# Performance work log

Measured on AMD Instinct MI355X. Metric: run time of the kernel, lower is better.

The kernel has to match this reference:

```python
import jax, jax.numpy as jnp
import numpy as np

ATTN_MULT = 8.0
NEG_INF = float('-inf')

N, Q, S, D = 16, 2048, 2048, 64


def setup_inputs() -> dict:
    key = jax.random.key(0)
    kq, kk, kv, kp = jax.random.split(key, 4)
    return {
        "queries_nqd": jax.random.normal(kq, (N, Q, D), dtype=jnp.float32),
        "keys_nsd": jax.random.normal(kk, (N, S, D), dtype=jnp.float32),
        "values_nsv": jax.random.normal(kv, (N, S, D), dtype=jnp.float32),
        "prefix_len_n": jax.random.randint(kp, (N,), 0, S, dtype=jnp.int64 if jax.config.jax_enable_x64 else jnp.int32),
    }


def reference(queries_nqd, keys_nsd, values_nsv, prefix_len_n):
    # attention_type == 'block_diagonal', backend == 'torch', dropout p == 0
    n, q, d = queries_nqd.shape
    s = keys_nsd.shape[1]
    scale = ATTN_MULT / d
    # prefix-block mask: key position < prefix_len (broadcast over queries)
    block_mask_n1s = (jnp.arange(s)[None, None, :] < prefix_len_n[:, None, None])  # [n,1,s]
    diag_mask_qs = jnp.arange(q)[:, None] == jnp.arange(s)[None, :]                # [q,s]
    mask_nqs = block_mask_n1s | diag_mask_qs[None, :, :]                           # [n,q,s]
    scores_nqs = jnp.einsum('nqd,nsd->nqs', queries_nqd, keys_nsd) * scale
    scores_nqs = jnp.where(mask_nqs, scores_nqs, NEG_INF)
    probs_nqs = jax.nn.softmax(scores_nqs, axis=-1)
    return jnp.einsum('nqs,nsv->nqv', probs_nqs, values_nsv)
```

## Files before the change

kernel.cpp:

```cpp
#include <hip/hip_runtime.h>
#include <hip/hip_bf16.h>
#include <math.h>

#define NH 16
#define QL 2048
#define SL 2048
#define DD 64
#define BQ 128
#define NSPLIT 2
#define PSTR 72
#define QK_SCALE_LOG2E 0.1803368801111f

typedef __attribute__((ext_vector_type(8))) short short8;
typedef __attribute__((ext_vector_type(4))) float floatx4;
typedef __attribute__((ext_vector_type(4))) unsigned short ushort4v;
typedef __attribute__((ext_vector_type(8))) unsigned short ushort8v;

__device__ __forceinline__ unsigned short f2bf(float x) {
    unsigned u = __float_as_uint(x);
    u += 0x7FFFu + ((u >> 16) & 1u);
    return (unsigned short)(u >> 16);
}
__device__ __forceinline__ unsigned int f2bf2u(float x, float y) {
    __hip_bfloat162 h = __float22bfloat162_rn(make_float2(x, y));
    return *(unsigned int*)&h;
}
__device__ __forceinline__ float bf2f(unsigned short h) {
    return __uint_as_float((unsigned)h << 16);
}

__device__ __forceinline__ void gld16(const unsigned short* g, unsigned short* l) {
    __builtin_amdgcn_global_load_lds(
        (const __attribute__((address_space(1))) unsigned int*)g,
        (__attribute__((address_space(3))) unsigned int*)l, 16, 0, 0);
}

__global__ __launch_bounds__(512) void k_prep(
    const float* __restrict__ Kf, const float* __restrict__ Vf,
    unsigned short* __restrict__ Kb, unsigned short* __restrict__ Vtb)
{
    __shared__ unsigned short sT[64][PSTR];
    const int bx = (int)blockIdx.x, tid = (int)threadIdx.x;

    const int gidx = bx * 512 + tid;
    #pragma unroll
    for (int k = 0; k < 2; ++k) {
        int idx = gidx + k * (512 * 512);
        float4 v = ((const float4*)Kf)[idx];
        ushort4v h = { f2bf(v.x), f2bf(v.y), f2bf(v.z), f2bf(v.w) };
        *(ushort4v*)(Kb + (size_t)idx * 4) = h;
    }

    const int n = bx >> 5, s0 = (bx & 31) * 64;
    const float* vb = Vf + ((size_t)n * SL + s0) * DD;
    #pragma unroll
    for (int i = 0; i < 2; ++i) {
        int idx = tid + i * 512;
        int r = idx >> 4, c = (idx & 15) << 2;
        float4 v = *(const float4*)(vb + r * DD + c);
        sT[c + 0][r] = f2bf(v.x);
        sT[c + 1][r] = f2bf(v.y);
        sT[c + 2][r] = f2bf(v.z);
        sT[c + 3][r] = f2bf(v.w);
    }
    __syncthreads();
    const int d = tid >> 3, sg = tid & 7;
    unsigned short* out = Vtb + (size_t)n * DD * SL + (size_t)d * SL + s0 + sg * 8;
    ushort8v a;
    #pragma unroll
    for (int i = 0; i < 8; ++i) a[i] = sT[d][sg * 8 + i];
    *(ushort8v*)out = a;
}

__global__ __launch_bounds__(512, 4) void k_attn(
    const float* __restrict__ Qf, const unsigned short* __restrict__ Kb,
    const unsigned short* __restrict__ Vtb, const int* __restrict__ plen_g,
    unsigned short* __restrict__ Opb, float* __restrict__ Lp)
{
    __shared__ unsigned short sK[3][64 * 64];
    __shared__ unsigned short sVt[3][64 * 64];
    __shared__ unsigned short sP[8 * 16 * 64];

    const int flat = (int)blockIdx.x;
    const int sp   = flat >> 8;
    const int rb   = flat & 255;
    const int n    = (rb + sp) & (NH - 1);
    const int qt   = rb >> 4;
    const int q0   = qt * BQ;
    const int plen = plen_g[n];

    const int tid  = (int)threadIdx.x;
    const int wave = tid >> 6, lane = tid & 63, quad = lane >> 4, l16 = lane & 15;

    const int ptiles = (plen + 63) >> 6;
    const int d0     = q0 >> 6;
    const int tdiag  = d0 + sp;
    const int cnt_p  = (ptiles + 1 - sp) >> 1;
    const int total  = cnt_p + (tdiag >= ptiles ? 1 : 0);

    const int qrow  = wave * 16 + l16;
    const int qglob = q0 + qrow;
    const int pmask = (l16 & 7) * 8;

    const unsigned short* kh = Kb  + (size_t)n * SL * DD;
    const unsigned short* vh = Vtb + (size_t)n * DD * SL;

    const int srow = wave * 8 + (lane >> 3);
    const int scol = ((lane & 7) ^ (srow & 7)) * 8;

    auto tile_of = [&](int i) -> int {
        return (i < cnt_p) ? (sp + (i << 1)) : tdiag;
    };
    auto stage = [&](int t, int b) {
        const unsigned short* kg = kh + ((size_t)t << 6) * DD;
        const unsigned short* vg = vh + (t << 6);
        gld16(kg + srow * DD + scol, sK[b] + wave * 512);
        gld16(vg + (size_t)srow * SL + scol, sVt[b] + wave * 512);
    };

    short8 bQ0, bQ1;
    {
        const float* qf = Qf + ((size_t)(n * QL + qglob)) * DD + quad * 8;
        float4 a0 = *(const float4*)(qf);
        float4 a1 = *(const float4*)(qf + 4);
        float4 c0 = *(const float4*)(qf + 32);
        float4 c1 = *(const float4*)(qf + 36);
        const float S = QK_SCALE_LOG2E;
        unsigned int u0[4] = {
            f2bf2u(a0.x * S, a0.y * S), f2bf2u(a0.z * S, a0.w * S),
            f2bf2u(a1.x * S, a1.y * S), f2bf2u(a1.z * S, a1.w * S) };
        unsigned int u1[4] = {
            f2bf2u(c0.x * S, c0.y * S), f2bf2u(c0.z * S, c0.w * S),
            f2bf2u(c1.x * S, c1.y * S), f2bf2u(c1.z * S, c1.w * S) };
        bQ0 = *(short8*)u0;
        bQ1 = *(short8*)u1;
    }

    stage(tile_of(0), 0);
    if (total > 1) stage(tile_of(1), 1);

    floatx4 acc[4];
    #pragma unroll
    for (int dt = 0; dt < 4; ++dt) acc[dt] = (floatx4){0.f, 0.f, 0.f, 0.f};
    float lsum = 0.f;
    unsigned short* pw = sP + qrow * 64;

    int bi = 0;
    int bs = 2;
    for (int i = 0; i < total; ++i) {
        if (i + 2 <= total) {
            asm volatile("s_waitcnt vmcnt(2) lgkmcnt(0)" ::: "memory");
        } else {
            asm volatile("s_waitcnt vmcnt(0) lgkmcnt(0)" ::: "memory");
        }
        __builtin_amdgcn_s_barrier();

        if (i + 2 < total) stage(tile_of(i + 2), bs);

        const unsigned short* sk = sK[bi];
        const unsigned short* sv = sVt[bi];
        const int t  = tile_of(i);
        const int s0 = t << 6;

        floatx4 sf[4];
        #pragma unroll
        for (int st2 = 0; st2 < 4; ++st2) sf[st2] = (floatx4){0.f, 0.f, 0.f, 0.f};
        __builtin_amdgcn_s_setprio(1);
        #pragma unroll
        for (int st2 = 0; st2 < 4; ++st2) {
            int krow = st2 * 16 + l16;
            short8 aK0 = *(const short8*)(sk + krow * 64 + (((0 * 4 + quad) ^ (krow & 7)) * 8));
            short8 aK1 = *(const short8*)(sk + krow * 64 + (((1 * 4 + quad) ^ (krow & 7)) * 8));
            sf[st2] = __builtin_amdgcn_mfma_f32_16x16x32_bf16(aK0, bQ0, sf[st2], 0, 0, 0);
            sf[st2] = __builtin_amdgcn_mfma_f32_16x16x32_bf16(aK1, bQ1, sf[st2], 0, 0, 0);
        }
        __builtin_amdgcn_s_setprio(0);

        if (s0 + 64 <= plen) {
            #pragma unroll
            for (int st2 = 0; st2 < 4; ++st2) {
                float p0 = __builtin_amdgcn_exp2f(sf[st2][0]);
                float p1 = __builtin_amdgcn_exp2f(sf[st2][1]);
                float p2 = __builtin_amdgcn_exp2f(sf[st2][2]);
                float p3 = __builtin_amdgcn_exp2f(sf[st2][3]);
                lsum += (p0 + p1) + (p2 + p3);
                uint2 pk = { f2bf2u(p0, p1), f2bf2u(p2, p3) };
                *(uint2*)(pw + ((st2 * 16 + quad * 4) ^ pmask)) = pk;
            }
        } else {
            #pragma unroll
            for (int st2 = 0; st2 < 4; ++st2) {
                float p[4];
                #pragma unroll
                for (int r2 = 0; r2 < 4; ++r2) {
                    int s = s0 + st2 * 16 + quad * 4 + r2;
                    bool valid = (s < plen) || (s == qglob);
                    p[r2] = __builtin_amdgcn_exp2f(valid ? sf[st2][r2] : -INFINITY);
                    lsum += p[r2];
                }
                uint2 pk = { f2bf2u(p[0], p[1]), f2bf2u(p[2], p[3]) };
                *(uint2*)(pw + ((st2 * 16 + quad * 4) ^ pmask)) = pk;
            }
        }

        __builtin_amdgcn_s_setprio(1);
        #pragma unroll
        for (int ks = 0; ks < 2; ++ks) {
            short8 aP = *(const short8*)(pw + ((ks * 32 + quad * 8) ^ pmask));
            #pragma unroll
            for (int dt = 0; dt < 4; ++dt) {
                int vrow = dt * 16 + l16;
                short8 bV = *(const short8*)(sv + vrow * 64 + (((ks * 4 + quad) ^ (vrow & 7)) * 8));
                acc[dt] = __builtin_amdgcn_mfma_f32_16x16x32_bf16(aP, bV, acc[dt], 0, 0, 0);
            }
        }
        __builtin_amdgcn_s_setprio(0);

        bi = (bi == 2) ? 0 : bi + 1;
        bs = (bs == 2) ? 0 : bs + 1;
    }

    lsum += __shfl_xor(lsum, 16, 64);
    lsum += __shfl_xor(lsum, 32, 64);
    if (quad == 0)
        Lp[((size_t)sp * NH + n) * QL + q0 + qrow] = lsum;

    unsigned short* pws = sP + wave * 16 * 64;
    #pragma unroll
    for (int dt = 0; dt < 4; ++dt) {
        int chunk = dt * 2 + (l16 >> 3);
        #pragma unroll
        for (int r2 = 0; r2 < 4; ++r2) {
            int row = quad * 4 + r2;
            int sw = ((chunk ^ (row & 7)) * 8) + (l16 & 7);
            pws[row * 64 + sw] = f2bf(acc[dt][r2]);
        }
    }
    const size_t qbase = ((size_t)sp * NH + n) * QL + q0 + wave * 16;
    #pragma unroll
    for (int t2 = 0; t2 < 2; ++t2) {
        int row = t2 * 8 + (lane >> 3);
        int chunk = lane & 7;
        int sw = (chunk ^ (row & 7)) * 8;
        ushort8v val = *(const ushort8v*)(pws + row * 64 + sw);
        *(ushort8v*)(Opb + (qbase + row) * DD + chunk * 8) = val;
    }
}

__global__ __launch_bounds__(512) void k_combine(
    const unsigned short* __restrict__ Opb, const float* __restrict__ Lp,
    float* __restrict__ Og)
{
    const int idx = (int)(blockIdx.x * 512 + threadIdx.x);
    const int d8 = idx & 7;
    const int q  = (idx >> 3) & (QL - 1);
    const int n  = idx >> 14;
    float s[8];
    #pragma unroll
    for (int j = 0; j < 8; ++j) s[j] = 0.f;
    float l = 0.f;
    #pragma unroll
    for (int sp = 0; sp < NSPLIT; ++sp) {
        const unsigned short* ob = Opb + (((size_t)sp * NH + n) * QL + q) * DD + d8 * 8;
        ushort8v v = *(const ushort8v*)ob;
        #pragma unroll
        for (int j = 0; j < 8; ++j) s[j] += bf2f(v[j]);
        l += Lp[((size_t)sp * NH + n) * QL + q];
    }
    const float inv = 1.0f / l;
    float4 o0 = { s[0] * inv, s[1] * inv, s[2] * inv, s[3] * inv };
    float4 o1 = { s[4] * inv, s[5] * inv, s[6] * inv, s[7] * inv };
    float* og = Og + ((size_t)n * QL + q) * DD + d8 * 8;
    *(float4*)og = o0;
    *(float4*)(og + 4) = o1;
}

extern "C" void kernel_launch(void* const* d_in, const int* in_sizes, int n_in,
                              void* d_out, int out_size, void* d_ws, size_t ws_size,
                              hipStream_t stream) {
    const float* Qf   = (const float*)d_in[0];
    const float* Kf   = (const float*)d_in[1];
    const float* Vf   = (const float*)d_in[2];
    const int*   plen = (const int*)d_in[3];
    float* Og = (float*)d_out;

    char* ws = (char*)d_ws;
    unsigned short* Kb  = (unsigned short*)(ws);
    unsigned short* Vtb = (unsigned short*)(ws + (4u << 20));
    unsigned short* Opb = (unsigned short*)(ws + (8u << 20));
    float*          Lp  = (float*)(ws + (16u << 20));

    k_prep<<<512, 512, 0, stream>>>(Kf, Vf, Kb, Vtb);
    k_attn<<<NSPLIT * 256, 512, 0, stream>>>(Qf, Kb, Vtb, plen, Opb, Lp);
    k_combine<<<512, 512, 0, stream>>>(Opb, Lp, Og);
}
```

Before: 104.4 us.

## Remove split-KV and combine kernel; normalize and write output directly

Drops the two-way split over key tiles. Each block now walks all prefix tiles plus its diagonal tiles, normalizes by the row sum in-kernel and writes fp32 output directly. This removes the combine kernel launch and the bf16 partial-output round trip through global memory. In exchange there are only 256 blocks, each with up to twice the serial work, which may leave the GPU underoccupied and worsen load imbalance, since prefix lengths vary per head.

Result: slower. 115.6 us (+10.8%).

```diff
diff --git a/kernel.cpp b/kernel.cpp
--- a/kernel.cpp
+++ b/kernel.cpp
@@ -7,7 +7,6 @@
 #define SL 2048
 #define DD 64
 #define BQ 128
-#define NSPLIT 2
 #define PSTR 72
 #define QK_SCALE_LOG2E 0.1803368801111f
 
@@ -75,17 +74,15 @@
 __global__ __launch_bounds__(512, 4) void k_attn(
     const float* __restrict__ Qf, const unsigned short* __restrict__ Kb,
     const unsigned short* __restrict__ Vtb, const int* __restrict__ plen_g,
-    unsigned short* __restrict__ Opb, float* __restrict__ Lp)
+    float* __restrict__ Og)
 {
     __shared__ unsigned short sK[3][64 * 64];
     __shared__ unsigned short sVt[3][64 * 64];
     __shared__ unsigned short sP[8 * 16 * 64];
 
-    const int flat = (int)blockIdx.x;
-    const int sp   = flat >> 8;
-    const int rb   = flat & 255;
-    const int n    = (rb + sp) & (NH - 1);
-    const int qt   = rb >> 4;
+    const int bx   = (int)blockIdx.x;
+    const int n    = bx & (NH - 1);
+    const int qt   = bx >> 4;
     const int q0   = qt * BQ;
     const int plen = plen_g[n];
 
@@ -94,9 +91,9 @@
 
     const int ptiles = (plen + 63) >> 6;
     const int d0     = q0 >> 6;
-    const int tdiag  = d0 + sp;
-    const int cnt_p  = (ptiles + 1 - sp) >> 1;
-    const int total  = cnt_p + (tdiag >= ptiles ? 1 : 0);
+    const int e0     = (d0 >= ptiles) ? 1 : 0;
+    const int e1     = (d0 + 1 >= ptiles) ? 1 : 0;
+    const int total  = ptiles + e0 + e1;
 
     const int qrow  = wave * 16 + l16;
     const int qglob = q0 + qrow;
@@ -109,7 +106,9 @@
     const int scol = ((lane & 7) ^ (srow & 7)) * 8;
 
     auto tile_of = [&](int i) -> int {
-        return (i < cnt_p) ? (sp + (i << 1)) : tdiag;
+        if (i < ptiles) return i;
+        if (i == ptiles) return e0 ? d0 : d0 + 1;
+        return d0 + 1;
     };
     auto stage = [&](int t, int b) {
         const unsigned short* kg = kh + ((size_t)t << 6) * DD;
@@ -222,57 +221,19 @@
 
     lsum += __shfl_xor(lsum, 16, 64);
     lsum += __shfl_xor(lsum, 32, 64);
-    if (quad == 0)
-        Lp[((size_t)sp * NH + n) * QL + q0 + qrow] = lsum;
-
-    unsigned short* pws = sP + wave * 16 * 64;
-    #pragma unroll
-    for (int dt = 0; dt < 4; ++dt) {
-        int chunk = dt * 2 + (l16 >> 3);
-        #pragma unroll
-        for (int r2 = 0; r2 < 4; ++r2) {
-            int row = quad * 4 + r2;
-            int sw = ((chunk ^ (row & 7)) * 8) + (l16 & 7);
-            pws[row * 64 + sw] = f2bf(acc[dt][r2]);
-        }
-    }
-    const size_t qbase = ((size_t)sp * NH + n) * QL + q0 + wave * 16;
-    #pragma unroll
-    for (int t2 = 0; t2 < 2; ++t2) {
-        int row = t2 * 8 + (lane >> 3);
-        int chunk = lane & 7;
-        int sw = (chunk ^ (row & 7)) * 8;
-        ushort8v val = *(const ushort8v*)(pws + row * 64 + sw);
-        *(ushort8v*)(Opb + (qbase + row) * DD + chunk * 8) = val;
-    }
-}
-
-__global__ __launch_bounds__(512) void k_combine(
-    const unsigned short* __restrict__ Opb, const float* __restrict__ Lp,
-    float* __restrict__ Og)
-{
-    const int idx = (int)(blockIdx.x * 512 + threadIdx.x);
-    const int d8 = idx & 7;
-    const int q  = (idx >> 3) & (QL - 1);
-    const int n  = idx >> 14;
-    float s[8];
-    #pragma unroll
-    for (int j = 0; j < 8; ++j) s[j] = 0.f;
-    float l = 0.f;
-    #pragma unroll
-    for (int sp = 0; sp < NSPLIT; ++sp) {
-        const unsigned short* ob = Opb + (((size_t)sp * NH + n) * QL + q) * DD + d8 * 8;
-        ushort8v v = *(const ushort8v*)ob;
-        #pragma unroll
-        for (int j = 0; j < 8; ++j) s[j] += bf2f(v[j]);
-        l += Lp[((size_t)sp * NH + n) * QL + q];
-    }
-    const float inv = 1.0f / l;
-    float4 o0 = { s[0] * inv, s[1] * inv, s[2] * inv, s[3] * inv };
-    float4 o1 = { s[4] * inv, s[5] * inv, s[6] * inv, s[7] * inv };
-    float* og = Og + ((size_t)n * QL + q) * DD + d8 * 8;
-    *(float4*)og = o0;
-    *(float4*)(og + 4) = o1;
+    float inv[4];
+    #pragma unroll
+    for (int r2 = 0; r2 < 4; ++r2)
+        inv[r2] = 1.0f / __shfl(lsum, quad * 4 + r2, 64);
+
+    float* ob = Og + ((size_t)n * QL + q0 + wave * 16) * DD + l16;
+    #pragma unroll
+    for (int r2 = 0; r2 < 4; ++r2) {
+        float* orow = ob + (quad * 4 + r2) * DD;
+        #pragma unroll
+        for (int dt = 0; dt < 4; ++dt)
+            orow[dt * 16] = acc[dt][r2] * inv[r2];
+    }
 }
 
 extern "C" void kernel_launch(void* const* d_in, const int* in_sizes, int n_in,
@@ -287,10 +248,7 @@
     char* ws = (char*)d_ws;
     unsigned short* Kb  = (unsigned short*)(ws);
     unsigned short* Vtb = (unsigned short*)(ws + (4u << 20));
-    unsigned short* Opb = (unsigned short*)(ws + (8u << 20));
-    float*          Lp  = (float*)(ws + (16u << 20));
 
     k_prep<<<512, 512, 0, stream>>>(Kf, Vf, Kb, Vtb);
-    k_attn<<<NSPLIT * 256, 512, 0, stream>>>(Qf, Kb, Vtb, plen, Opb, Lp);
-    k_combine<<<512, 512, 0, stream>>>(Opb, Lp, Og);
-}
+    k_attn<<<NH * (QL / BQ), 512, 0, stream>>>(Qf, Kb, Vtb, plen, Og);
+}
```
